# Performance work log

Measured on AMD Instinct MI355X. Metric: run time of the kernel, lower is better.

The kernel has to match this reference:

```python
import jax, jax.numpy as jnp
import numpy as np

B, N, M, F, K = 32, 256, 64, 128, 64
N_INTERACT_RES, N_ATOM_RES = 3, 2


def ssp(x):
    # shifted softplus, PhysNet activation
    return jax.nn.softplus(x) - jnp.log(2.0).astype(x.dtype)


def res_block(h, W1, b1, W2, b2):
    # PhysNet residual layer: h + W2 @ ssp(W1 @ ssp(h) + b1) + b2
    t = ssp(h)
    t = ssp(t @ W1.T + b1)
    return h + t @ W2.T + b2


def setup_inputs() -> dict:
    key = jax.random.key(0)
    ks = jax.random.split(key, 20)
    sF = 1.0 / np.sqrt(F)
    sK = 1.0 / np.sqrt(K)
    return {
        "x": jax.random.normal(ks[0], (B, N, F), jnp.float32),
        "rbf": jax.random.uniform(ks[1], (B, N, M, K), jnp.float32),
        "neighbor": jax.random.randint(ks[2], (B, N, M), 0, N, jnp.int32),
        "k2f_W": jax.random.normal(ks[3], (F, K), jnp.float32) * sK,  # no bias
        "Wi": jax.random.normal(ks[4], (F, F), jnp.float32) * sF,
        "bi": jnp.zeros((F,), jnp.float32),
        "ires_W1": jax.random.normal(ks[5], (N_INTERACT_RES, F, F), jnp.float32) * sF,
        "ires_b1": jnp.zeros((N_INTERACT_RES, F), jnp.float32),
        "ires_W2": jax.random.normal(ks[6], (N_INTERACT_RES, F, F), jnp.float32) * sF,
        "ires_b2": jnp.zeros((N_INTERACT_RES, F), jnp.float32),
        "Wint": jax.random.normal(ks[7], (F, F), jnp.float32) * sF,
        "bint": jnp.zeros((F,), jnp.float32),
        "u_gate": jnp.ones((F,), jnp.float32),
        "ares_W1": jax.random.normal(ks[8], (N_ATOM_RES, F, F), jnp.float32) * sF,
        "ares_b1": jnp.zeros((N_ATOM_RES, F), jnp.float32),
        "ares_W2": jax.random.normal(ks[9], (N_ATOM_RES, F, F), jnp.float32) * sF,
        "ares_b2": jnp.zeros((N_ATOM_RES, F), jnp.float32),
    }


def reference(x, rbf, neighbor, k2f_W, Wi, bi, ires_W1, ires_b1, ires_W2, ires_b2,
              Wint, bint, u_gate, ares_W1, ares_b1, ares_W2, ares_b2):
    b, n, f = x.shape
    m = neighbor.shape[2]
    xa = ssp(x)                                            # (B,N,F)
    g = jnp.einsum('bnmk,fk->bnmf', rbf, k2f_W)            # RBF filter (B,N,M,F)
    xi = ssp(xa @ Wi.T + bi)                               # self message
    # gather neighbor features: xj[b,n,m,:] = xa[b, neighbor[b,n,m], :]
    idx = jnp.broadcast_to(neighbor.reshape(b, n * m)[:, :, None], (b, n * m, f))
    xj = jnp.take_along_axis(xa, idx, axis=1).reshape(b, n, m, f)
    xj = jnp.sum(xj * g, axis=2)                           # aggregate over neighbors
    v = xi + xj
    for l in range(ires_W1.shape[0]):
        v = res_block(v, ires_W1[l], ires_b1[l], ires_W2[l], ires_b2[l])
    v = ssp(v)
    out = u_gate * x + (v @ Wint.T + bint)
    for l in range(ares_W1.shape[0]):
        out = res_block(out, ares_W1[l], ares_b1[l], ares_W2[l], ares_b2[l])
    return out
```

## Files before the change

### kernel.cpp

```cpp
#include <hip/hip_runtime.h>
#include <math.h>

#define PB 32
#define PN 256
#define PM 64
#define PF 128
#define PK 64
#define ROWS (PB*PN)
#define NTOT (ROWS*PF)

#define OFF_K2F  0
#define OFF_WI   8192
#define OFF_IW1  24576
#define OFF_IW2  73728
#define OFF_WINT 122880
#define OFF_AW1  139264
#define OFF_AW2  172032
#define TOTAL_W  204800

#define XPITCH 136
#define GPITCH 132

#define APB 32

typedef __attribute__((ext_vector_type(4))) float  floatx4;
typedef __attribute__((ext_vector_type(8))) short  shortx8;

__device__ __forceinline__ unsigned short f2b(float f){
    union { float f; unsigned int i; } c; c.f = f;
    unsigned int x = c.i;
    return (unsigned short)((x + 0x7fffu + ((x >> 16) & 1u)) >> 16);
}
__device__ __forceinline__ float sspf(float x){
    const float LOG2E = 1.4426950408889634f;
    const float LN2   = 0.6931471805599453f;
    float t = __builtin_amdgcn_exp2f(-fabsf(x) * LOG2E);
    return fmaxf(x, 0.0f) + LN2 * __builtin_amdgcn_logf(1.0f + t) - LN2;
}
__device__ __forceinline__ shortx8 pack8(float4 a, float4 b){
    shortx8 r;
    r[0]=(short)f2b(a.x); r[1]=(short)f2b(a.y); r[2]=(short)f2b(a.z); r[3]=(short)f2b(a.w);
    r[4]=(short)f2b(b.x); r[5]=(short)f2b(b.y); r[6]=(short)f2b(b.z); r[7]=(short)f2b(b.w);
    return r;
}

__global__ __launch_bounds__(256) void k_pre(const float* __restrict__ x,
                                             const float* __restrict__ k2f,
                                             const float* __restrict__ Wi,
                                             const float* __restrict__ iW1,
                                             const float* __restrict__ iW2,
                                             const float* __restrict__ Wint,
                                             const float* __restrict__ aW1,
                                             const float* __restrict__ aW2,
                                             float* __restrict__ xa_f,
                                             unsigned short* __restrict__ xa_b,
                                             unsigned short* __restrict__ Wb){
    int i = blockIdx.x * 256 + threadIdx.x;
    if (i < NTOT){
        float v = sspf(x[i]);
        xa_f[i] = v;
        xa_b[i] = f2b(v);
        return;
    }
    int j = i - NTOT;
    if (j >= TOTAL_W) return;
    float v;
    if      (j < OFF_WI)   v = k2f[j - OFF_K2F];
    else if (j < OFF_IW1)  v = Wi[j - OFF_WI];
    else if (j < OFF_IW2)  v = iW1[j - OFF_IW1];
    else if (j < OFF_WINT) v = iW2[j - OFF_IW2];
    else if (j < OFF_AW1)  v = Wint[j - OFF_WINT];
    else if (j < OFF_AW2)  v = aW1[j - OFF_AW1];
    else                   v = aW2[j - OFF_AW2];
    Wb[j] = f2b(v);
}

__global__ __launch_bounds__(512, 2) void k_msg(const float* __restrict__ rbf,
                                                const int* __restrict__ nbr,
                                                const unsigned short* __restrict__ Wk2f,
                                                const float* __restrict__ xa_f,
                                                float* __restrict__ xj){
    const int tid  = threadIdx.x;
    const int w    = tid >> 6;
    const int lane = tid & 63;
    const int quad = lane >> 4;
    const int l16  = lane & 15;

    const int blk   = blockIdx.x;
    const int b     = blk >> 3;
    const int atom0 = b * PN + (blk & 7) * APB;
    const int awave = atom0 + w*4;

    __shared__ float xa_s[PN * GPITCH];

    const int rboff = l16 * PK + quad*8;
    const float* rb_base = rbf + (size_t)awave * (PM*PK);
    const int*   nb_base = nbr + (size_t)awave * PM + quad*4;

    float4 pA0,pA1,pA2,pA3, pB0,pB1,pB2,pB3;
    int4 nbA, nbB;
    {
        const float* p0 = rb_base + rboff;
        pA0 = *(const float4*)(p0);
        pA1 = *(const float4*)(p0 + 4);
        pA2 = *(const float4*)(p0 + 32);
        pA3 = *(const float4*)(p0 + 36);
        nbA = *(const int4*)(nb_base);
        const float* p1 = rb_base + 16*PK + rboff;
        pB0 = *(const float4*)(p1);
        pB1 = *(const float4*)(p1 + 4);
        pB2 = *(const float4*)(p1 + 32);
        pB3 = *(const float4*)(p1 + 36);
        nbB = *(const int4*)(nb_base + 16);
    }

    shortx8 bf0[8], bf1[8];
    #pragma unroll
    for (int ft = 0; ft < 8; ++ft){
        const unsigned short* wrow = Wk2f + (size_t)(ft*16 + l16) * PK;
        bf0[ft] = *(const shortx8*)(wrow + quad*8);
        bf1[ft] = *(const shortx8*)(wrow + 32 + quad*8);
    }

    const float* src = xa_f + (size_t)b * (PN*PF);
    #pragma unroll
    for (int p = 0; p < 16; ++p){
        int idx = p*2048 + tid*4;
        int row = idx >> 7, col = idx & 127;
        *(float4*)(&xa_s[row*GPITCH + col]) = *(const float4*)(src + idx);
    }
    __syncthreads();

    float s[8];
    #pragma unroll
    for (int it = 0; it < 16; ++it){
        const int ai = it >> 2;
        const int t  = it & 3;

        shortx8 af0, af1; int4 nb;
        if ((it & 1) == 0){ af0 = pack8(pA0,pA1); af1 = pack8(pA2,pA3); nb = nbA; }
        else              { af0 = pack8(pB0,pB1); af1 = pack8(pB2,pB3); nb = nbB; }

        if (it + 2 < 16){
            const int it2 = it + 2;
            const int ai2 = it2 >> 2, t2 = it2 & 3;
            const float* pn = rb_base + (size_t)ai2*(PM*PK) + t2*16*PK + rboff;
            const int4*  nn = (const int4*)(nb_base + (size_t)ai2*PM + t2*16);
            if ((it & 1) == 0){
                pA0 = *(const float4*)(pn);
                pA1 = *(const float4*)(pn + 4);
                pA2 = *(const float4*)(pn + 32);
                pA3 = *(const float4*)(pn + 36);
                nbA = *nn;
            } else {
                pB0 = *(const float4*)(pn);
                pB1 = *(const float4*)(pn + 4);
                pB2 = *(const float4*)(pn + 32);
                pB3 = *(const float4*)(pn + 36);
                nbB = *nn;
            }
        }

        floatx4 acc8[8];
        #pragma unroll
        for (int ft = 0; ft < 8; ++ft){
            floatx4 c = {0.f, 0.f, 0.f, 0.f};
            c = __builtin_amdgcn_mfma_f32_16x16x32_bf16(af0, bf0[ft], c, 0, 0, 0);
            c = __builtin_amdgcn_mfma_f32_16x16x32_bf16(af1, bf1[ft], c, 0, 0, 0);
            acc8[ft] = c;
        }

        const float* rp0 = xa_s + (size_t)nb.x*GPITCH + l16;
        const float* rp1 = xa_s + (size_t)nb.y*GPITCH + l16;
        const float* rp2 = xa_s + (size_t)nb.z*GPITCH + l16;
        const float* rp3 = xa_s + (size_t)nb.w*GPITCH + l16;
        #pragma unroll
        for (int ft = 0; ft < 8; ++ft){
            float v =  acc8[ft][0] * rp0[ft*16];
            v       += acc8[ft][1] * rp1[ft*16];
            v       += acc8[ft][2] * rp2[ft*16];
            v       += acc8[ft][3] * rp3[ft*16];
            if (t == 0) s[ft] = v; else s[ft] += v;
        }

        if (t == 3){
            #pragma unroll
            for (int ft = 0; ft < 8; ++ft){
                float v = s[ft];
                v += __shfl_xor(v, 16, 64);
                v += __shfl_xor(v, 32, 64);
                if (quad == 0) xj[(size_t)(awave + ai)*PF + ft*16 + l16] = v;
            }
        }
    }
}

__device__ __forceinline__ void lw8(const unsigned short* __restrict__ W,
                                    int l16, int quad, int ftb, shortx8 wf[8]){
    #pragma unroll
    for (int f = 0; f < 2; ++f)
        #pragma unroll
        for (int ks = 0; ks < 4; ++ks)
            wf[f*4+ks] = *(const shortx8*)(W + (size_t)((ftb+f)*16 + l16)*PF + ks*32 + quad*8);
}
__device__ __forceinline__ void gemm2p(const shortx8 wf[8], const shortx8 a[4], floatx4 acc[2]){
    #pragma unroll
    for (int f = 0; f < 2; ++f){
        floatx4 c = {0.f, 0.f, 0.f, 0.f};
        #pragma unroll
        for (int ks = 0; ks < 4; ++ks)
            c = __builtin_amdgcn_mfma_f32_16x16x32_bf16(a[ks], wf[f*4+ks], c, 0, 0, 0);
        acc[f] = c;
    }
}

__device__ __forceinline__ void relayout(unsigned short* Tls,
                                         const unsigned short t16[8],
                                         int l16, int quad, int ftbase,
                                         shortx8 a[4]){
    #pragma unroll
    for (int f = 0; f < 2; ++f)
        #pragma unroll
        for (int r = 0; r < 4; ++r)
            Tls[(quad*4 + r)*XPITCH + (ftbase+f)*16 + l16] = t16[f*4 + r];
    __syncthreads();
    #pragma unroll
    for (int ks = 0; ks < 4; ++ks)
        a[ks] = *(const shortx8*)(Tls + l16*XPITCH + ks*32 + quad*8);
}

__global__ __launch_bounds__(256) void k_chain(const unsigned short* __restrict__ xa_b,
                                               const float* __restrict__ xj,
                                               const float* __restrict__ x,
                                               const unsigned short* __restrict__ Wb,
                                               const float* __restrict__ bi,
                                               const float* __restrict__ ib1,
                                               const float* __restrict__ ib2,
                                               const float* __restrict__ bint,
                                               const float* __restrict__ ugate,
                                               const float* __restrict__ ab1,
                                               const float* __restrict__ ab2,
                                               float* __restrict__ out){
    const int tid  = threadIdx.x;
    const int wave = tid >> 6;
    const int lane = tid & 63;
    const int quad = lane >> 4;
    const int l16  = lane & 15;
    const int ftb  = wave*2;
    const int row0 = blockIdx.x * 16;

    __shared__ unsigned short Tls[2][16 * XPITCH];
    int p = 0;

    int col[2];
    #pragma unroll
    for (int f = 0; f < 2; ++f) col[f] = (ftb+f)*16 + l16;

    const unsigned short* inrow = xa_b + (size_t)(row0 + l16) * PF;
    shortx8 a[4];
    #pragma unroll
    for (int ks = 0; ks < 4; ++ks)
        a[ks] = *(const shortx8*)(inrow + ks*32 + quad*8);

    shortx8 wA[8], wB[8];
    lw8(Wb + OFF_WI, l16, quad, ftb, wA);

    floatx4 acc[2];
    float V[8];
    unsigned short t16[8];

    lw8(Wb + OFF_IW1, l16, quad, ftb, wB);
    gemm2p(wA, a, acc);
    #pragma unroll
    for (int f = 0; f < 2; ++f)
        #pragma unroll
        for (int r = 0; r < 4; ++r){
            size_t idx = (size_t)(row0 + quad*4 + r)*PF + col[f];
            float of = sspf(acc[f][r] + bi[col[f]]) + xj[idx];
            V[f*4+r] = of;
            t16[f*4+r] = f2b(sspf(of));
        }
    relayout(Tls[p], t16, l16, quad, ftb, a); p ^= 1;

    #pragma unroll
    for (int l = 0; l < 3; ++l){
        lw8(Wb + OFF_IW2 + l*PF*PF, l16, quad, ftb, wA);
        gemm2p(wB, a, acc);
        #pragma unroll
        for (int f = 0; f < 2; ++f)
            #pragma unroll
            for (int r = 0; r < 4; ++r)
                t16[f*4+r] = f2b(sspf(acc[f][r] + ib1[l*PF + col[f]]));
        relayout(Tls[p], t16, l16, quad, ftb, a); p ^= 1;

        lw8(Wb + (l < 2 ? OFF_IW1 + (l+1)*PF*PF : OFF_WINT), l16, quad, ftb, wB);
        gemm2p(wA, a, acc);
        #pragma unroll
        for (int f = 0; f < 2; ++f)
            #pragma unroll
            for (int r = 0; r < 4; ++r){
                V[f*4+r] += acc[f][r] + ib2[l*PF + col[f]];
                t16[f*4+r] = f2b(sspf(V[f*4+r]));
            }
        relayout(Tls[p], t16, l16, quad, ftb, a); p ^= 1;
    }

    lw8(Wb + OFF_AW1, l16, quad, ftb, wA);
    gemm2p(wB, a, acc);
    #pragma unroll
    for (int f = 0; f < 2; ++f)
        #pragma unroll
        for (int r = 0; r < 4; ++r){
            size_t idx = (size_t)(row0 + quad*4 + r)*PF + col[f];
            float o = ugate[col[f]] * x[idx] + acc[f][r] + bint[col[f]];
            V[f*4+r] = o;
            t16[f*4+r] = f2b(sspf(o));
        }
    relayout(Tls[p], t16, l16, quad, ftb, a); p ^= 1;

    #pragma unroll
    for (int l = 0; l < 2; ++l){
        lw8(Wb + OFF_AW2 + l*PF*PF, l16, quad, ftb, wB);
        gemm2p(wA, a, acc);
        #pragma unroll
        for (int f = 0; f < 2; ++f)
            #pragma unroll
            for (int r = 0; r < 4; ++r)
                t16[f*4+r] = f2b(sspf(acc[f][r] + ab1[l*PF + col[f]]));
        relayout(Tls[p], t16, l16, quad, ftb, a); p ^= 1;

        if (l == 0) lw8(Wb + OFF_AW1 + PF*PF, l16, quad, ftb, wA);
        gemm2p(wB, a, acc);
        if (l == 0){
            #pragma unroll
            for (int f = 0; f < 2; ++f)
                #pragma unroll
                for (int r = 0; r < 4; ++r){
                    V[f*4+r] += acc[f][r] + ab2[l*PF + col[f]];
                    t16[f*4+r] = f2b(sspf(V[f*4+r]));
                }
            relayout(Tls[p], t16, l16, quad, ftb, a); p ^= 1;
        } else {
            #pragma unroll
            for (int f = 0; f < 2; ++f)
                #pragma unroll
                for (int r = 0; r < 4; ++r){
                    size_t idx = (size_t)(row0 + quad*4 + r)*PF + col[f];
                    out[idx] = V[f*4+r] + acc[f][r] + ab2[l*PF + col[f]];
                }
        }
    }
}

extern "C" void kernel_launch(void* const* d_in, const int* in_sizes, int n_in,
                              void* d_out, int out_size, void* d_ws, size_t ws_size,
                              hipStream_t stream){
    const float* x     = (const float*)d_in[0];
    const float* rbf   = (const float*)d_in[1];
    const int*   nbr   = (const int*)d_in[2];
    const float* k2fW  = (const float*)d_in[3];
    const float* Wi    = (const float*)d_in[4];
    const float* bi    = (const float*)d_in[5];
    const float* iW1   = (const float*)d_in[6];
    const float* ib1   = (const float*)d_in[7];
    const float* iW2   = (const float*)d_in[8];
    const float* ib2   = (const float*)d_in[9];
    const float* Wint  = (const float*)d_in[10];
    const float* bint  = (const float*)d_in[11];
    const float* ugate = (const float*)d_in[12];
    const float* aW1   = (const float*)d_in[13];
    const float* ab1   = (const float*)d_in[14];
    const float* aW2   = (const float*)d_in[15];
    const float* ab2   = (const float*)d_in[16];

    char* ws = (char*)d_ws;
    unsigned short* xa_b = (unsigned short*)ws;
    float*          xa_f = (float*)(ws + (2ull  << 20));
    float*          xj   = (float*)(ws + (6ull  << 20));
    unsigned short* Wb   = (unsigned short*)(ws + (10ull << 20));

    k_pre<<<(NTOT + TOTAL_W + 255)/256, 256, 0, stream>>>(
        x, k2fW, Wi, iW1, iW2, Wint, aW1, aW2, xa_f, xa_b, Wb);
    k_msg<<<PB * (PN/APB), 512, 0, stream>>>(rbf, nbr, Wb + OFF_K2F, xa_f, xj);
    k_chain<<<ROWS/16, 256, 0, stream>>>(xa_b, xj, x, Wb,
                                         bi, ib1, ib2, bint, ugate, ab1, ab2,
                                         (float*)d_out);
}
```

Measured before the change: 300.9 us.

## Stage k2f weights in LDS and shrink rbf prefetch to single buffer

The message kernel now stages the bf16 k2f weight fragments in shared memory, in MFMA lane order, instead of holding 16 shortx8 fragments per thread in registers. The rbf/neighbor prefetch drops from two buffered tiles to one tile ahead. The MFMA and neighbor-gather loops are fused so each filter column is consumed right after it is computed. The aim is to cut VGPR pressure and possible spills, at the cost of extra LDS reads every iteration and less latency hiding for the dominant rbf stream.

After: 272.4 us. 1.1x faster.

```diff
diff --git a/kernel.cpp b/kernel.cpp
--- a/kernel.cpp
+++ b/kernel.cpp
@@ -91,35 +91,31 @@
     const int atom0 = b * PN + (blk & 7) * APB;
     const int awave = atom0 + w*4;
 
-    __shared__ float xa_s[PN * GPITCH];
+    __shared__ float          xa_s[PN * GPITCH];
+    __shared__ unsigned short w_s[8192];
 
     const int rboff = l16 * PK + quad*8;
     const float* rb_base = rbf + (size_t)awave * (PM*PK);
     const int*   nb_base = nbr + (size_t)awave * PM + quad*4;
 
-    float4 pA0,pA1,pA2,pA3, pB0,pB1,pB2,pB3;
-    int4 nbA, nbB;
+    float4 r0, r1, r2, r3; int4 nb;
     {
         const float* p0 = rb_base + rboff;
-        pA0 = *(const float4*)(p0);
-        pA1 = *(const float4*)(p0 + 4);
-        pA2 = *(const float4*)(p0 + 32);
-        pA3 = *(const float4*)(p0 + 36);
-        nbA = *(const int4*)(nb_base);
-        const float* p1 = rb_base + 16*PK + rboff;
-        pB0 = *(const float4*)(p1);
-        pB1 = *(const float4*)(p1 + 4);
-        pB2 = *(const float4*)(p1 + 32);
-        pB3 = *(const float4*)(p1 + 36);
-        nbB = *(const int4*)(nb_base + 16);
-    }
-
-    shortx8 bf0[8], bf1[8];
-    #pragma unroll
-    for (int ft = 0; ft < 8; ++ft){
-        const unsigned short* wrow = Wk2f + (size_t)(ft*16 + l16) * PK;
-        bf0[ft] = *(const shortx8*)(wrow + quad*8);
-        bf1[ft] = *(const shortx8*)(wrow + 32 + quad*8);
+        r0 = *(const float4*)(p0);
+        r1 = *(const float4*)(p0 + 4);
+        r2 = *(const float4*)(p0 + 32);
+        r3 = *(const float4*)(p0 + 36);
+        nb = *(const int4*)(nb_base);
+    }
+
+    #pragma unroll
+    for (int rep = 0; rep < 2; ++rep){
+        int f  = rep*512 + tid;
+        int s  = f >> 9;
+        int ft = (f >> 6) & 7;
+        int ln = f & 63;
+        const unsigned short* g = Wk2f + (size_t)(ft*16 + (ln & 15))*PK + s*32 + (ln >> 4)*8;
+        *(shortx8*)(&w_s[f*8]) = *(const shortx8*)(g);
     }
 
     const float* src = xa_f + (size_t)b * (PN*PF);
@@ -137,49 +133,37 @@
         const int ai = it >> 2;
         const int t  = it & 3;
 
-        shortx8 af0, af1; int4 nb;
-        if ((it & 1) == 0){ af0 = pack8(pA0,pA1); af1 = pack8(pA2,pA3); nb = nbA; }
-        else              { af0 = pack8(pB0,pB1); af1 = pack8(pB2,pB3); nb = nbB; }
-
-        if (it + 2 < 16){
-            const int it2 = it + 2;
+        shortx8 af0 = pack8(r0, r1);
+        shortx8 af1 = pack8(r2, r3);
+        const int4 nbc = nb;
+
+        if (it + 1 < 16){
+            const int it2 = it + 1;
             const int ai2 = it2 >> 2, t2 = it2 & 3;
             const float* pn = rb_base + (size_t)ai2*(PM*PK) + t2*16*PK + rboff;
-            const int4*  nn = (const int4*)(nb_base + (size_t)ai2*PM + t2*16);
-            if ((it & 1) == 0){
-                pA0 = *(const float4*)(pn);
-                pA1 = *(const float4*)(pn + 4);
-                pA2 = *(const float4*)(pn + 32);
-                pA3 = *(const float4*)(pn + 36);
-                nbA = *nn;
-            } else {
-                pB0 = *(const float4*)(pn);
-                pB1 = *(const float4*)(pn + 4);
-                pB2 = *(const float4*)(pn + 32);
-                pB3 = *(const float4*)(pn + 36);
-                nbB = *nn;
-            }
-        }
-
-        floatx4 acc8[8];
+            r0 = *(const float4*)(pn);
+            r1 = *(const float4*)(pn + 4);
+            r2 = *(const float4*)(pn + 32);
+            r3 = *(const float4*)(pn + 36);
+            nb = *(const int4*)(nb_base + (size_t)ai2*PM + t2*16);
+        }
+
+        const float* rp0 = xa_s + (size_t)nbc.x*GPITCH + l16;
+        const float* rp1 = xa_s + (size_t)nbc.y*GPITCH + l16;
+        const float* rp2 = xa_s + (size_t)nbc.z*GPITCH + l16;
+        const float* rp3 = xa_s + (size_t)nbc.w*GPITCH + l16;
+
         #pragma unroll
         for (int ft = 0; ft < 8; ++ft){
+            shortx8 b0 = *(const shortx8*)(&w_s[(ft*64 + lane)*8]);
+            shortx8 b1 = *(const shortx8*)(&w_s[((8 + ft)*64 + lane)*8]);
             floatx4 c = {0.f, 0.f, 0.f, 0.f};
-            c = __builtin_amdgcn_mfma_f32_16x16x32_bf16(af0, bf0[ft], c, 0, 0, 0);
-            c = __builtin_amdgcn_mfma_f32_16x16x32_bf16(af1, bf1[ft], c, 0, 0, 0);
-            acc8[ft] = c;
-        }
-
-        const float* rp0 = xa_s + (size_t)nb.x*GPITCH + l16;
-        const float* rp1 = xa_s + (size_t)nb.y*GPITCH + l16;
-        const float* rp2 = xa_s + (size_t)nb.z*GPITCH + l16;
-        const float* rp3 = xa_s + (size_t)nb.w*GPITCH + l16;
-        #pragma unroll
-        for (int ft = 0; ft < 8; ++ft){
-            float v =  acc8[ft][0] * rp0[ft*16];
-            v       += acc8[ft][1] * rp1[ft*16];
-            v       += acc8[ft][2] * rp2[ft*16];
-            v       += acc8[ft][3] * rp3[ft*16];
+            c = __builtin_amdgcn_mfma_f32_16x16x32_bf16(af0, b0, c, 0, 0, 0);
+            c = __builtin_amdgcn_mfma_f32_16x16x32_bf16(af1, b1, c, 0, 0, 0);
+            float v =  c[0] * rp0[ft*16];
+            v       += c[1] * rp1[ft*16];
+            v       += c[2] * rp2[ft*16];
+            v       += c[3] * rp3[ft*16];
             if (t == 0) s[ft] = v; else s[ft] += v;
         }
 
```
